# Performance work log

Hardware: AMD Instinct MI355X
Metric: run time of the kernel (lower is better)

The kernel has to match this reference:

```python
import jax, jax.numpy as jnp
import numpy as np

T, B, S = 8, 4, 2048
LAT, SYM, NC = 1024, 256, 512


def setup_inputs() -> dict:
    key = jax.random.key(0)
    ks = jax.random.split(key, 16)
    inp = {
        "token_state": jax.random.normal(ks[0], (B, S, LAT), jnp.float32),
        "bus_symbols": jax.random.normal(ks[1], (T, B, S, SYM), jnp.float32),
        "bus_indices": jax.random.randint(ks[2], (T, B, S), 0, NC),
        "bus_outputs": jax.random.normal(ks[3], (T, B, S, LAT), jnp.float32),
        "bus_mask": jnp.zeros((T,), jnp.bool_),
        # parameters (stored as (in, out) matrices)
        "Wq": jax.random.normal(ks[4], (SYM, 1), jnp.float32) / np.sqrt(SYM),
        "bq": jnp.zeros((1,), jnp.float32),
        "Wread": jax.random.normal(ks[5], (2 * LAT, LAT), jnp.float32) / np.sqrt(2 * LAT),
        "bread": jnp.zeros((LAT,), jnp.float32),
        "Wsym": jax.random.normal(ks[6], (LAT, SYM), jnp.float32) / np.sqrt(LAT),
        "bsym": jnp.zeros((SYM,), jnp.float32),
        "Wc1": jax.random.normal(ks[7], (LAT + SYM, LAT), jnp.float32) / np.sqrt(LAT + SYM),
        "bc1": jnp.zeros((LAT,), jnp.float32),
        "Wc2": jax.random.normal(ks[8], (LAT, LAT), jnp.float32) / np.sqrt(LAT),
        "bc2": jnp.zeros((LAT,), jnp.float32),
        "codebook": jax.random.normal(ks[9], (NC, SYM), jnp.float32),
    }
    return inp


def reference(token_state, bus_symbols, bus_indices, bus_outputs, bus_mask,
              Wq, bq, Wread, bread, Wsym, bsym, Wc1, bc1, Wc2, bc2, codebook):
    Tm, Bb, Ss, Dsym = bus_symbols.shape
    N = Bb * Ss
    syms = bus_symbols.reshape(Tm, N, Dsym)          # [T, N, SYM]
    outs = bus_outputs.reshape(Tm, N, -1)            # [T, N, LAT]

    # top-1 bus message routing
    relevance = (syms @ Wq + bq)[..., 0]             # [T, N]
    top_msg_idx = jnp.argmax(relevance, axis=0)      # [N]
    chosen = jnp.take_along_axis(outs, top_msg_idx[None, :, None], axis=0)[0]  # [N, LAT]
    bus_context = chosen.reshape(Bb, Ss, -1)

    z = jnp.concatenate([token_state, bus_context], axis=-1)
    z_read = z @ Wread + bread                       # [B, S, LAT]
    raw_symbol = z_read @ Wsym + bsym                # [B, S, SYM]

    # VQ: cdist argmin (squared distance has same argmin)
    flat = raw_symbol.reshape(-1, Dsym)              # [N, SYM]
    d2 = (jnp.sum(flat * flat, axis=1, keepdims=True)
          - 2.0 * flat @ codebook.T
          + jnp.sum(codebook * codebook, axis=1)[None, :])  # [N, NC]
    indices = jnp.argmin(d2, axis=-1)                # [N]
    quantized = codebook[indices].reshape(Bb, Ss, Dsym)

    h = jax.nn.relu(jnp.concatenate([z_read, quantized], axis=-1) @ Wc1 + bc1)
    node_output = h @ Wc2 + bc2 + token_state

    used_counts = jnp.zeros((Tm,), jnp.int32).at[top_msg_idx].add(1)
    keep_mask = used_counts == 0
    return node_output, quantized, indices.reshape(Bb, Ss), keep_mask
```

## Files before the change

### kernel.cpp

```cpp
#include <hip/hip_runtime.h>
#include <hip/hip_bf16.h>

#define DEVI __device__ __forceinline__

namespace {

constexpr int T_   = 8;
constexpr int NTOK = 8192;
constexpr int LAT  = 1024;
constexpr int SYM  = 256;
constexpr int NC   = 512;
constexpr float TAU = 0.6f;

typedef short short8 __attribute__((ext_vector_type(8)));
typedef float floatx4 __attribute__((ext_vector_type(4)));

DEVI unsigned short f2bf(float f){
  union { float f; unsigned u; } v; v.f = f;
  return (unsigned short)((v.u + 0x7fffu + ((v.u >> 16) & 1u)) >> 16);
}

DEVI void gload_lds16(const void* g, void* l){
  __builtin_amdgcn_global_load_lds((const __attribute__((address_space(1))) void*)g,
                                   (__attribute__((address_space(3))) void*)l, 16, 0, 0);
}

__global__ void route_k(const float* __restrict__ syms, const float* __restrict__ Wq,
                        int* __restrict__ top, int* __restrict__ counts){
  int gt = blockIdx.x * blockDim.x + threadIdx.x;
  int wid = gt >> 6, lane = gt & 63;
  if (wid >= NTOK) return;
  float4 wq = *(const float4*)(Wq + lane * 4);
  float best = -INFINITY; int bt = 0;
  for (int t = 0; t < T_; ++t){
    float4 s = *(const float4*)(syms + ((size_t)t * NTOK + wid) * SYM + lane * 4);
    float p = s.x*wq.x + s.y*wq.y + s.z*wq.z + s.w*wq.w;
    #pragma unroll
    for (int off = 32; off; off >>= 1) p += __shfl_down(p, off, 64);
    p = __shfl(p, 0, 64);
    if (p > best){ best = p; bt = t; }
  }
  if (lane == 0){ top[wid] = bt; atomicAdd(&counts[bt], 1); }
}

__global__ void cbt_k(const float* __restrict__ cb, float* __restrict__ cbT,
                      const int* __restrict__ counts, float* __restrict__ out_mask){
  int i = blockIdx.x * blockDim.x + threadIdx.x;
  if (i < NC * SYM){ int c = i / SYM, k = i % SYM; cbT[k * NC + c] = cb[i]; }
  if (blockIdx.x == 0 && threadIdx.x < T_)
    out_mask[threadIdx.x] = (counts[threadIdx.x] == 0) ? 1.0f : 0.0f;
}

__global__ void cnorm_k(const float* __restrict__ cb, const float* __restrict__ bsym,
                        float* __restrict__ cnorm, float* __restrict__ svec,
                        const float* __restrict__ bread, const float* __restrict__ Wsym,
                        float* __restrict__ rb){
  if (blockIdx.x == NC/4){
    int t = threadIdx.x;
    float a0=0.f,a1=0.f,a2=0.f,a3=0.f;
    for (int k = 0; k < LAT; k += 4){
      a0 += bread[k+0] * Wsym[(size_t)(k+0) * SYM + t];
      a1 += bread[k+1] * Wsym[(size_t)(k+1) * SYM + t];
      a2 += bread[k+2] * Wsym[(size_t)(k+2) * SYM + t];
      a3 += bread[k+3] * Wsym[(size_t)(k+3) * SYM + t];
    }
    rb[t] = bsym[t] + ((a0+a1)+(a2+a3));
    return;
  }
  int gt = blockIdx.x * blockDim.x + threadIdx.x;
  int wid = gt >> 6, lane = gt & 63;
  if (wid >= NC) return;
  float4 v = *(const float4*)(cb + (size_t)wid * SYM + lane * 4);
  float4 b = *(const float4*)(bsym + lane * 4);
  float p = v.x*v.x + v.y*v.y + v.z*v.z + v.w*v.w;
  float q = v.x*(v.x-2.f*b.x) + v.y*(v.y-2.f*b.y) + v.z*(v.z-2.f*b.z) + v.w*(v.w-2.f*b.w);
  #pragma unroll
  for (int off = 32; off; off >>= 1){ p += __shfl_down(p, off, 64); q += __shfl_down(q, off, 64); }
  if (lane == 0){ cnorm[wid] = p; svec[wid] = q; }
}

__global__ void t32multi_k(const float* __restrict__ Wread, unsigned short* __restrict__ WreadT,
                           const float* __restrict__ Wc1,   unsigned short* __restrict__ Wc1T,
                           const float* __restrict__ Wc2,   unsigned short* __restrict__ Wc2T){
  __shared__ float tile[32][33];
  int b = blockIdx.x;
  const float* in; unsigned short* out; int R, C, t;
  if (b < 2048){ in = Wread; out = WreadT; R = 2*LAT; C = LAT; t = b; }
  else if (b < 2048+1280){ in = Wc1; out = Wc1T; R = LAT+SYM; C = LAT; t = b - 2048; }
  else { in = Wc2; out = Wc2T; R = LAT; C = LAT; t = b - 3328; }
  int bx = t % 32, by = t / 32;
  int r0 = by * 32, c0 = bx * 32;
  int tid = threadIdx.x;
  int tx = tid & 31, ty = tid >> 5;
  #pragma unroll
  for (int j = 0; j < 4; ++j)
    tile[ty + j*8][tx] = in[(size_t)(r0 + ty + j*8) * C + c0 + tx];
  __syncthreads();
  #pragma unroll
  for (int j = 0; j < 4; ++j)
    out[(size_t)(c0 + ty + j*8) * R + r0 + tx] = f2bf(tile[tx][ty + j*8]);
}

__global__ void pack_az(const float* __restrict__ ts, const float* __restrict__ bus,
                        const int* __restrict__ top, unsigned short* __restrict__ Az){
  int id = blockIdx.x * blockDim.x + threadIdx.x;
  int m = id >> 9, c = (id & 511) * 4;
  const float* src = (c < LAT) ? (ts + (size_t)m * LAT + c)
                               : (bus + ((size_t)top[m] * NTOK + m) * LAT + (c - LAT));
  float4 v = *(const float4*)src;
  ushort4 o; o.x = f2bf(v.x); o.y = f2bf(v.y); o.z = f2bf(v.z); o.w = f2bf(v.w);
  *(ushort4*)(Az + (size_t)m * (2*LAT) + c) = o;
}

template<int BM, int BN, int BK, int TM, int TN, int TB>
__global__ __launch_bounds__((BM/TM)*(BN/TN))
void gemm_f32(const float* __restrict__ A, const float* __restrict__ Bm,
              float* __restrict__ Cf, unsigned short* __restrict__ Ct,
              int M, int N, int K)
{
  constexpr int NT  = (BM/TM)*(BN/TN);
  constexpr int BMp = BM + 4, BNp = BN + 4;
  constexpr int KV  = BK / 4;
  constexpr int NLA = BM * KV;
  constexpr int NLB = (BK * BN) / 4;
  __shared__ float As[BK][BMp];
  __shared__ float Bs[BK][BNp];
  const int tid = threadIdx.x;
  const int tx = tid % (BN / TN), ty = tid / (BN / TN);
  const int m0 = blockIdx.x * BM, n0 = blockIdx.y * BN;
  float acc[TM][TN] = {};
  for (int k0 = 0; k0 < K; k0 += BK){
    for (int q = tid; q < NLA; q += NT){
      int m = q / KV, kq = (q % KV) * 4;
      float4 v = *(const float4*)(A + (size_t)(m0+m) * K + k0 + kq);
      As[kq+0][m] = v.x; As[kq+1][m] = v.y; As[kq+2][m] = v.z; As[kq+3][m] = v.w;
    }
    for (int q = tid; q < NLB; q += NT){
      int k = q / (BN/4), n4 = (q % (BN/4)) * 4;
      *(float4*)&Bs[k][n4] = *(const float4*)(Bm + (size_t)(k0+k) * N + n0 + n4);
    }
    __syncthreads();
    #pragma unroll
    for (int k = 0; k < BK; ++k){
      float a[TM], b[TN];
      #pragma unroll
      for (int i = 0; i < TM; ++i) a[i] = As[k][ty*TM + i];
      #pragma unroll
      for (int j = 0; j < TN; ++j) b[j] = Bs[k][tx*TN + j];
      #pragma unroll
      for (int i = 0; i < TM; ++i)
        #pragma unroll
        for (int j = 0; j < TN; ++j) acc[i][j] += a[i] * b[j];
    }
    __syncthreads();
  }
  #pragma unroll
  for (int i = 0; i < TM; ++i)
    #pragma unroll
    for (int j = 0; j < TN; ++j){
      if constexpr (TB){
        Ct[(size_t)(n0 + tx*TN + j) * M + m0 + ty*TM + i] = f2bf(acc[i][j]);
      } else {
        Cf[(size_t)(m0 + ty*TM + i) * N + n0 + tx*TN + j] = acc[i][j];
      }
    }
}

constexpr int A_PLAIN = 0, A_CAT = 1;
constexpr int EP_ZH = 0, EP_VQ = 1, EP_RELU = 2, EP_OUT = 3;

template<int ASRC, int EPI>
__global__ __launch_bounds__(256)
void mgemm(const unsigned short* __restrict__ A, const unsigned short* __restrict__ A2,
           const unsigned short* __restrict__ BT, const float* __restrict__ bias,
           const float* __restrict__ resid,
           unsigned short* __restrict__ Cb, float* __restrict__ Cf,
           int N, int K, int asplit)
{
  __shared__ unsigned short As[128*32];
  __shared__ unsigned short Bs[128*32];
  const int tid  = threadIdx.x;
  const int wave = tid >> 6, lane = tid & 63;
  const int wy = wave >> 1, wx = wave & 1;
  const int lq = lane >> 4, lr = lane & 15;

  const int nwg  = gridDim.x * gridDim.y;
  const int orig = blockIdx.y * gridDim.x + blockIdx.x;
  const int dec  = (orig & 7) * (nwg >> 3) + (orig >> 3);
  const int bx   = dec % gridDim.x, by = dec / gridDim.x;
  const int m0 = by * 128, n0 = bx * 128;

  floatx4 acc[4][4] = {};

  for (int k0 = 0; k0 < K; k0 += 32){
    #pragma unroll
    for (int c = 0; c < 2; ++c){
      int chunk = tid + c*256;
      int mrel = chunk >> 2, kc = (chunk & 3) * 8;
      int gk = k0 + kc;
      const unsigned short* srcA;
      if constexpr (ASRC == A_CAT){
        if (gk < asplit) srcA = A  + (size_t)(m0+mrel) * asplit + gk;
        else             srcA = A2 + (size_t)(m0+mrel) * (K-asplit) + (gk-asplit);
      } else {
        srcA = A + (size_t)(m0+mrel) * K + gk;
      }
      gload_lds16(srcA, &As[(c*256 + wave*64) * 8]);
      gload_lds16(BT + (size_t)(n0+mrel) * K + gk, &Bs[(c*256 + wave*64) * 8]);
    }
    __syncthreads();
    short8 af[4], bf[4];
    #pragma unroll
    for (int i = 0; i < 4; ++i){
      af[i] = *(const short8*)&As[(wy*64 + i*16 + lr)*32 + lq*8];
      bf[i] = *(const short8*)&Bs[(wx*64 + i*16 + lr)*32 + lq*8];
    }
    #pragma unroll
    for (int i = 0; i < 4; ++i)
      #pragma unroll
      for (int j = 0; j < 4; ++j)
        acc[i][j] = __builtin_amdgcn_mfma_f32_16x16x32_bf16(af[i], bf[j], acc[i][j], 0, 0, 0);
    __syncthreads();
  }

  #pragma unroll
  for (int i = 0; i < 4; ++i){
    #pragma unroll
    for (int j = 0; j < 4; ++j){
      int gn = n0 + wx*64 + j*16 + lr;
      #pragma unroll
      for (int r = 0; r < 4; ++r){
        int gm = m0 + wy*64 + i*16 + lq*4 + r;
        float v = acc[i][j][r];
        if constexpr (EPI == EP_ZH){
          Cb[(size_t)gm * N + gn] = f2bf(v + bias[gn]);
        } else if constexpr (EPI == EP_VQ){
          Cf[(size_t)gm * N + gn] = bias[gn] - 2.f * v;
        } else if constexpr (EPI == EP_RELU){
          float u = v + bias[gn];
          Cb[(size_t)gm * N + gn] = f2bf(u > 0.f ? u : 0.f);
        } else {
          Cf[(size_t)gm * N + gn] = v + bias[gn] + resid[(size_t)gm * N + gn];
        }
      }
    }
  }
}

__global__ void vq_k(const float* __restrict__ scores, const float* __restrict__ cb,
                     float* __restrict__ out_q, float* __restrict__ out_idx,
                     unsigned short* __restrict__ q_h,
                     int* __restrict__ rcount, int* __restrict__ rlist){
  int gt = blockIdx.x * blockDim.x + threadIdx.x;
  int wid = gt >> 6, lane = gt & 63;
  if (wid >= NTOK) return;
  const float* row = scores + (size_t)wid * NC;
  float v1 = INFINITY, v2 = INFINITY; int i1 = 0x7fffffff;
  #pragma unroll
  for (int i = 0; i < NC/64; ++i){
    int c = i*64 + lane;
    float v = row[c];
    if (v < v1){ v2 = v1; v1 = v; i1 = c; } else v2 = fminf(v2, v);
  }
  #pragma unroll
  for (int off = 32; off; off >>= 1){
    float ov1 = __shfl_down(v1, off, 64);
    int   oi1 = __shfl_down(i1, off, 64);
    float ov2 = __shfl_down(v2, off, 64);
    float rest;
    if (ov1 < v1 || (ov1 == v1 && oi1 < i1)){ rest = v1; v1 = ov1; i1 = oi1; }
    else rest = ov1;
    v2 = fminf(fminf(v2, ov2), rest);
  }
  i1 = __shfl(i1, 0, 64);
  if (lane == 0){
    out_idx[wid] = (float)i1;
    if (__shfl(v2, 0, 64) - __shfl(v1, 0, 64) < TAU){
      int p = atomicAdd(rcount, 1); rlist[p] = wid;
    }
  }
  float4 cv = *(const float4*)(cb + (size_t)i1 * SYM + lane * 4);
  *(float4*)(out_q + (size_t)wid * SYM + lane * 4) = cv;
  ushort4 qh; qh.x = f2bf(cv.x); qh.y = f2bf(cv.y); qh.z = f2bf(cv.z); qh.w = f2bf(cv.w);
  *(ushort4*)(q_h + (size_t)wid * SYM + lane * 4) = qh;
}

constexpr int RT = 4;

__global__ __launch_bounds__(256)
void repair_k(const int* __restrict__ rcount, const int* __restrict__ rlist,
              const int* __restrict__ top,
              const float* __restrict__ ts, const float* __restrict__ bus,
              const float* __restrict__ Wcomb, const float* __restrict__ rb,
              const float* __restrict__ cb, const float* __restrict__ cnorm,
              float* __restrict__ out_q, float* __restrict__ out_idx,
              unsigned short* __restrict__ q_h){
  __shared__ float a[RT][2*LAT];
  __shared__ float raw[RT][SYM];
  __shared__ float pv[RT][4];
  __shared__ int   pi[RT][4];
  __shared__ int   fidx[RT];
  int tid = threadIdx.x;
  int lane = tid & 63, wave = tid >> 6;
  int cnt = *rcount;
  int nchunk = (cnt + RT - 1) / RT;
  for (int ch = blockIdx.x; ch < nchunk; ch += gridDim.x){
    int base = ch * RT;
    int nt = min(RT, cnt - base);
    for (int q = tid; q < nt * 512; q += 256){
      int t = q >> 9, c = (q & 511) * 4;
      int m = rlist[base + t];
      int tp = top[m];
      float4 v = (c < LAT) ? *(const float4*)(ts + (size_t)m * LAT + c)
                           : *(const float4*)(bus + ((size_t)tp * NTOK + m) * LAT + (c - LAT));
      *(float4*)&a[t][c] = v;
    }
    __syncthreads();
    float acc0[RT], acc1[RT], acc2[RT], acc3[RT];
    #pragma unroll
    for (int t = 0; t < RT; ++t){ acc0[t]=0.f; acc1[t]=0.f; acc2[t]=0.f; acc3[t]=0.f; }
    for (int k = 0; k < 2*LAT; k += 4){
      float w0 = Wcomb[(size_t)(k+0) * SYM + tid];
      float w1 = Wcomb[(size_t)(k+1) * SYM + tid];
      float w2 = Wcomb[(size_t)(k+2) * SYM + tid];
      float w3 = Wcomb[(size_t)(k+3) * SYM + tid];
      #pragma unroll
      for (int t = 0; t < RT; ++t){
        float4 av = *(const float4*)&a[t][k];
        acc0[t] += av.x * w0; acc1[t] += av.y * w1;
        acc2[t] += av.z * w2; acc3[t] += av.w * w3;
      }
    }
    #pragma unroll
    for (int t = 0; t < RT; ++t)
      raw[t][tid] = rb[tid] + ((acc0[t] + acc1[t]) + (acc2[t] + acc3[t]));
    __syncthreads();
    float bv[RT]; int bi[RT];
    #pragma unroll
    for (int t = 0; t < RT; ++t){ bv[t] = INFINITY; bi[t] = 0x7fffffff; }
    #pragma unroll
    for (int cc = 0; cc < 2; ++cc){
      int c = tid + cc * 256;
      const float* cr = cb + (size_t)c * SYM;
      float d[RT] = {};
      for (int j = 0; j < SYM; j += 4){
        float4 cv = *(const float4*)(cr + j);
        #pragma unroll
        for (int t = 0; t < RT; ++t){
          float4 rv4 = *(const float4*)&raw[t][j];
          d[t] += rv4.x*cv.x + rv4.y*cv.y + rv4.z*cv.z + rv4.w*cv.w;
        }
      }
      #pragma unroll
      for (int t = 0; t < RT; ++t){
        float s = cnorm[c] - 2.f * d[t];
        if (s < bv[t] || (s == bv[t] && c < bi[t])){ bv[t] = s; bi[t] = c; }
      }
    }
    #pragma unroll
    for (int t = 0; t < RT; ++t){
      float v = bv[t]; int i = bi[t];
      #pragma unroll
      for (int off = 32; off; off >>= 1){
        float ov = __shfl_down(v, off, 64);
        int   oi = __shfl_down(i, off, 64);
        if (ov < v || (ov == v && oi < i)){ v = ov; i = oi; }
      }
      if (lane == 0){ pv[t][wave] = v; pi[t][wave] = i; }
    }
    __syncthreads();
    if (tid < nt){
      float v = pv[tid][0]; int i = pi[tid][0];
      #pragma unroll
      for (int w = 1; w < 4; ++w){
        if (pv[tid][w] < v || (pv[tid][w] == v && pi[tid][w] < i)){ v = pv[tid][w]; i = pi[tid][w]; }
      }
      fidx[tid] = i;
      out_idx[rlist[base + tid]] = (float)i;
    }
    __syncthreads();
    for (int t = 0; t < nt; ++t){
      int m = rlist[base + t];
      int idx = fidx[t];
      float cvv = cb[(size_t)idx * SYM + tid];
      out_q[(size_t)m * SYM + tid] = cvv;
      q_h[(size_t)m * SYM + tid] = f2bf(cvv);
    }
    __syncthreads();
  }
}

}

extern "C" void kernel_launch(void* const* d_in, const int* in_sizes, int n_in,
                              void* d_out, int out_size, void* d_ws, size_t ws_size,
                              hipStream_t stream){
  const float* token_state = (const float*)d_in[0];
  const float* bus_symbols = (const float*)d_in[1];
  const float* bus_outputs = (const float*)d_in[3];
  const float* Wq    = (const float*)d_in[5];
  const float* Wread = (const float*)d_in[7];
  const float* bread = (const float*)d_in[8];
  const float* Wsym  = (const float*)d_in[9];
  const float* bsym  = (const float*)d_in[10];
  const float* Wc1   = (const float*)d_in[11];
  const float* bc1   = (const float*)d_in[12];
  const float* Wc2   = (const float*)d_in[13];
  const float* bc2   = (const float*)d_in[14];
  const float* codebook = (const float*)d_in[15];

  float* out_node = (float*)d_out;
  float* out_quant= out_node + (size_t)NTOK * LAT;
  float* out_idx  = out_quant + (size_t)NTOK * SYM;
  float* out_mask = out_idx + NTOK;

  char* W = (char*)d_ws; size_t off = 0;
  auto alloc = [&](size_t bytes)->char*{ char* p = W + off; off = (off + bytes + 255) & ~(size_t)255; return p; };
  int*   top     = (int*)alloc(NTOK*4);
  char*  zeroed  = alloc(256);
  int*   counts  = (int*)zeroed;
  int*   rcount  = (int*)(zeroed + 128);
  int*   rlist   = (int*)alloc(NTOK*4);
  float* cbT     = (float*)alloc((size_t)SYM*NC*4);
  float* cnorm   = (float*)alloc(NC*4);
  float* svec    = (float*)alloc(NC*4);
  float* rb      = (float*)alloc(SYM*4);
  float* Wcomb   = (float*)alloc((size_t)2*LAT*SYM*4);
  unsigned short* WreadT = (unsigned short*)alloc((size_t)LAT*2*LAT*2);
  unsigned short* Wc1T   = (unsigned short*)alloc((size_t)LAT*(LAT+SYM)*2);
  unsigned short* Wc2T   = (unsigned short*)alloc((size_t)LAT*LAT*2);
  unsigned short* WfuseT = (unsigned short*)alloc((size_t)NC*LAT*2);
  unsigned short* z_h    = (unsigned short*)alloc((size_t)NTOK*LAT*2);
  unsigned short* q_h    = (unsigned short*)alloc((size_t)NTOK*SYM*2);
  unsigned short* h_h    = (unsigned short*)alloc((size_t)NTOK*LAT*2);
  char* az_region        = alloc((size_t)NTOK*2*LAT*2);
  unsigned short* A_z    = (unsigned short*)az_region;
  float* scores          = (float*)az_region;

  hipMemsetAsync(zeroed, 0, 256, stream);

  route_k<<<NTOK/4, 256, 0, stream>>>(bus_symbols, Wq, top, counts);
  cbt_k<<<(NC*SYM)/256, 256, 0, stream>>>(codebook, cbT, counts, out_mask);
  cnorm_k<<<NC/4 + 1, 256, 0, stream>>>(codebook, bsym, cnorm, svec, bread, Wsym, rb);

  gemm_f32<64,64,8,4,4,1><<<dim3(LAT/64, NC/64), 256, 0, stream>>>(
      Wsym, cbT, nullptr, WfuseT, LAT, NC, SYM);
  gemm_f32<32,64,8,2,4,0><<<dim3(2*LAT/32, SYM/64), 256, 0, stream>>>(
      Wread, Wsym, Wcomb, nullptr, 2*LAT, SYM, LAT);
  t32multi_k<<<2048+1280+1024, 256, 0, stream>>>(Wread, WreadT, Wc1, Wc1T, Wc2, Wc2T);

  pack_az<<<(NTOK*512)/256, 256, 0, stream>>>(token_state, bus_outputs, top, A_z);

  mgemm<A_PLAIN, EP_ZH><<<dim3(LAT/128, NTOK/128), 256, 0, stream>>>(
      A_z, nullptr, WreadT, bread, nullptr, z_h, nullptr, LAT, 2*LAT, 0);
  mgemm<A_PLAIN, EP_VQ><<<dim3(NC/128, NTOK/128), 256, 0, stream>>>(
      z_h, nullptr, WfuseT, svec, nullptr, nullptr, scores, NC, LAT, 0);

  vq_k<<<NTOK/4, 256, 0, stream>>>(scores, codebook, out_quant, out_idx, q_h, rcount, rlist);
  repair_k<<<512, 256, 0, stream>>>(rcount, rlist, top, token_state, bus_outputs,
                                    Wcomb, rb, codebook, cnorm, out_quant, out_idx, q_h);

  mgemm<A_CAT, EP_RELU><<<dim3(LAT/128, NTOK/128), 256, 0, stream>>>(
      z_h, q_h, Wc1T, bc1, nullptr, h_h, nullptr, LAT, LAT+SYM, LAT);
  mgemm<A_PLAIN, EP_OUT><<<dim3(LAT/128, NTOK/128), 256, 0, stream>>>(
      h_h, nullptr, Wc2T, bc2, token_state, nullptr, out_node, LAT, LAT, 0);
}
```

Baseline: 905.9 us.

## Fuse routing with A-pack and merge weight-prep kernels into one launch

Routing now packs each token's bf16 A row (token state plus chosen bus output) in the same wave, so the separate pack kernel and its re-read of top indices go away. All weight preprocessing (Wfuse GEMM reading the codebook directly without a transposed copy, Wcomb GEMM, the three transposes, codebook norms, read bias) is merged into one block-dispatched kernel. The keep-mask write moves into the VQ kernel. This cuts launch count and lets the small prep jobs run side by side, at the cost of uneven per-block work and strided codebook loads in the Wfuse tile.

```diff
diff --git a/kernel.cpp b/kernel.cpp
--- a/kernel.cpp
+++ b/kernel.cpp
@@ -25,11 +25,12 @@
                                    (__attribute__((address_space(3))) void*)l, 16, 0, 0);
 }
 
-__global__ void route_k(const float* __restrict__ syms, const float* __restrict__ Wq,
-                        int* __restrict__ top, int* __restrict__ counts){
+__global__ void routepack_k(const float* __restrict__ syms, const float* __restrict__ Wq,
+                            const float* __restrict__ ts, const float* __restrict__ bus,
+                            int* __restrict__ top, int* __restrict__ counts,
+                            unsigned short* __restrict__ Az){
   int gt = blockIdx.x * blockDim.x + threadIdx.x;
   int wid = gt >> 6, lane = gt & 63;
-  if (wid >= NTOK) return;
   float4 wq = *(const float4*)(Wq + lane * 4);
   float best = -INFINITY; int bt = 0;
   for (int t = 0; t < T_; ++t){
@@ -41,35 +42,126 @@
     if (p > best){ best = p; bt = t; }
   }
   if (lane == 0){ top[wid] = bt; atomicAdd(&counts[bt], 1); }
-}
-
-__global__ void cbt_k(const float* __restrict__ cb, float* __restrict__ cbT,
-                      const int* __restrict__ counts, float* __restrict__ out_mask){
-  int i = blockIdx.x * blockDim.x + threadIdx.x;
-  if (i < NC * SYM){ int c = i / SYM, k = i % SYM; cbT[k * NC + c] = cb[i]; }
-  if (blockIdx.x == 0 && threadIdx.x < T_)
-    out_mask[threadIdx.x] = (counts[threadIdx.x] == 0) ? 1.0f : 0.0f;
-}
-
-__global__ void cnorm_k(const float* __restrict__ cb, const float* __restrict__ bsym,
-                        float* __restrict__ cnorm, float* __restrict__ svec,
-                        const float* __restrict__ bread, const float* __restrict__ Wsym,
-                        float* __restrict__ rb){
-  if (blockIdx.x == NC/4){
-    int t = threadIdx.x;
-    float a0=0.f,a1=0.f,a2=0.f,a3=0.f;
-    for (int k = 0; k < LAT; k += 4){
-      a0 += bread[k+0] * Wsym[(size_t)(k+0) * SYM + t];
-      a1 += bread[k+1] * Wsym[(size_t)(k+1) * SYM + t];
-      a2 += bread[k+2] * Wsym[(size_t)(k+2) * SYM + t];
-      a3 += bread[k+3] * Wsym[(size_t)(k+3) * SYM + t];
-    }
-    rb[t] = bsym[t] + ((a0+a1)+(a2+a3));
-    return;
-  }
-  int gt = blockIdx.x * blockDim.x + threadIdx.x;
-  int wid = gt >> 6, lane = gt & 63;
-  if (wid >= NC) return;
+  const float* tsrow  = ts  + (size_t)wid * LAT;
+  const float* busrow = bus + ((size_t)bt * NTOK + wid) * LAT;
+  unsigned short* az  = Az + (size_t)wid * (2*LAT);
+  #pragma unroll
+  for (int i = 0; i < 4; ++i){
+    int c = (i*64 + lane) * 4;
+    float4 v = *(const float4*)(tsrow + c);
+    ushort4 o; o.x = f2bf(v.x); o.y = f2bf(v.y); o.z = f2bf(v.z); o.w = f2bf(v.w);
+    *(ushort4*)(az + c) = o;
+    float4 w = *(const float4*)(busrow + c);
+    ushort4 p2; p2.x = f2bf(w.x); p2.y = f2bf(w.y); p2.z = f2bf(w.z); p2.w = f2bf(w.w);
+    *(ushort4*)(az + LAT + c) = p2;
+  }
+}
+
+constexpr int MP_WFUSE = 128, MP_WCOMB = 384, MP_T32 = 4736, MP_CNORM = 4864;
+
+DEVI void dev_wfuse(int tb, int tid, float* smem,
+                    const float* __restrict__ Wsym, const float* __restrict__ cb,
+                    unsigned short* __restrict__ WfuseT){
+  float (*As)[68] = (float(*)[68])smem;
+  float (*Bs)[68] = (float(*)[68])(smem + 544);
+  const int bxm = tb & 15, byn = tb >> 4;
+  const int m0 = bxm * 64, n0 = byn * 64;
+  const int tx = tid & 15, ty = tid >> 4;
+  float acc[4][4] = {};
+  for (int k0 = 0; k0 < SYM; k0 += 8){
+    if (tid < 128){
+      int m = tid >> 1, kq = (tid & 1) * 4;
+      float4 v = *(const float4*)(Wsym + (size_t)(m0+m) * SYM + k0 + kq);
+      As[kq+0][m] = v.x; As[kq+1][m] = v.y; As[kq+2][m] = v.z; As[kq+3][m] = v.w;
+    }
+    {
+      int n = tid >> 2, kk = (tid & 3) * 2;
+      float2 v = *(const float2*)(cb + (size_t)(n0+n) * SYM + k0 + kk);
+      Bs[kk+0][n] = v.x; Bs[kk+1][n] = v.y;
+    }
+    __syncthreads();
+    #pragma unroll
+    for (int k = 0; k < 8; ++k){
+      float a[4], b[4];
+      #pragma unroll
+      for (int i = 0; i < 4; ++i) a[i] = As[k][ty*4 + i];
+      #pragma unroll
+      for (int j = 0; j < 4; ++j) b[j] = Bs[k][tx*4 + j];
+      #pragma unroll
+      for (int i = 0; i < 4; ++i)
+        #pragma unroll
+        for (int j = 0; j < 4; ++j) acc[i][j] += a[i] * b[j];
+    }
+    __syncthreads();
+  }
+  #pragma unroll
+  for (int i = 0; i < 4; ++i)
+    #pragma unroll
+    for (int j = 0; j < 4; ++j)
+      WfuseT[(size_t)(n0 + tx*4 + j) * LAT + m0 + ty*4 + i] = f2bf(acc[i][j]);
+}
+
+DEVI void dev_wcomb(int tb, int tid, float* smem,
+                    const float* __restrict__ Wread, const float* __restrict__ Wsym,
+                    float* __restrict__ Wcomb){
+  float (*As)[68] = (float(*)[68])smem;
+  float (*Bs)[68] = (float(*)[68])(smem + 544);
+  const int bxm = tb & 63, byn = tb >> 6;
+  const int m0 = bxm * 32, n0 = byn * 64;
+  const int tx = tid & 15, ty = tid >> 4;
+  float acc[2][4] = {};
+  for (int k0 = 0; k0 < LAT; k0 += 8){
+    if (tid < 64){
+      int m = tid >> 1, kq = (tid & 1) * 4;
+      float4 v = *(const float4*)(Wread + (size_t)(m0+m) * LAT + k0 + kq);
+      As[kq+0][m] = v.x; As[kq+1][m] = v.y; As[kq+2][m] = v.z; As[kq+3][m] = v.w;
+    }
+    if (tid < 128){
+      int k = tid >> 4, n4 = (tid & 15) * 4;
+      *(float4*)&Bs[k][n4] = *(const float4*)(Wsym + (size_t)(k0+k) * SYM + n0 + n4);
+    }
+    __syncthreads();
+    #pragma unroll
+    for (int k = 0; k < 8; ++k){
+      float a[2], b[4];
+      #pragma unroll
+      for (int i = 0; i < 2; ++i) a[i] = As[k][ty*2 + i];
+      #pragma unroll
+      for (int j = 0; j < 4; ++j) b[j] = Bs[k][tx*4 + j];
+      #pragma unroll
+      for (int i = 0; i < 2; ++i)
+        #pragma unroll
+        for (int j = 0; j < 4; ++j) acc[i][j] += a[i] * b[j];
+    }
+    __syncthreads();
+  }
+  #pragma unroll
+  for (int i = 0; i < 2; ++i)
+    #pragma unroll
+    for (int j = 0; j < 4; ++j)
+      Wcomb[(size_t)(m0 + ty*2 + i) * SYM + n0 + tx*4 + j] = acc[i][j];
+}
+
+DEVI void dev_t32(int t, int tid, float* smem,
+                  const float* __restrict__ in, unsigned short* __restrict__ out,
+                  int R, int C){
+  float (*tile)[33] = (float(*)[33])smem;
+  int bx = t % 32, by = t / 32;
+  int r0 = by * 32, c0 = bx * 32;
+  int tx = tid & 31, ty = tid >> 5;
+  #pragma unroll
+  for (int j = 0; j < 4; ++j)
+    tile[ty + j*8][tx] = in[(size_t)(r0 + ty + j*8) * C + c0 + tx];
+  __syncthreads();
+  #pragma unroll
+  for (int j = 0; j < 4; ++j)
+    out[(size_t)(c0 + ty + j*8) * R + r0 + tx] = f2bf(tile[tx][ty + j*8]);
+}
+
+DEVI void dev_cnorm(int lb, int tid, const float* __restrict__ cb,
+                    const float* __restrict__ bsym,
+                    float* __restrict__ cnorm, float* __restrict__ svec){
+  int wid = lb * 4 + (tid >> 6), lane = tid & 63;
   float4 v = *(const float4*)(cb + (size_t)wid * SYM + lane * 4);
   float4 b = *(const float4*)(bsym + lane * 4);
   float p = v.x*v.x + v.y*v.y + v.z*v.z + v.w*v.w;
@@ -79,91 +171,45 @@
   if (lane == 0){ cnorm[wid] = p; svec[wid] = q; }
 }
 
-__global__ void t32multi_k(const float* __restrict__ Wread, unsigned short* __restrict__ WreadT,
-                           const float* __restrict__ Wc1,   unsigned short* __restrict__ Wc1T,
-                           const float* __restrict__ Wc2,   unsigned short* __restrict__ Wc2T){
-  __shared__ float tile[32][33];
-  int b = blockIdx.x;
-  const float* in; unsigned short* out; int R, C, t;
-  if (b < 2048){ in = Wread; out = WreadT; R = 2*LAT; C = LAT; t = b; }
-  else if (b < 2048+1280){ in = Wc1; out = Wc1T; R = LAT+SYM; C = LAT; t = b - 2048; }
-  else { in = Wc2; out = Wc2T; R = LAT; C = LAT; t = b - 3328; }
-  int bx = t % 32, by = t / 32;
-  int r0 = by * 32, c0 = bx * 32;
-  int tid = threadIdx.x;
-  int tx = tid & 31, ty = tid >> 5;
-  #pragma unroll
-  for (int j = 0; j < 4; ++j)
-    tile[ty + j*8][tx] = in[(size_t)(r0 + ty + j*8) * C + c0 + tx];
-  __syncthreads();
-  #pragma unroll
-  for (int j = 0; j < 4; ++j)
-    out[(size_t)(c0 + ty + j*8) * R + r0 + tx] = f2bf(tile[tx][ty + j*8]);
-}
-
-__global__ void pack_az(const float* __restrict__ ts, const float* __restrict__ bus,
-                        const int* __restrict__ top, unsigned short* __restrict__ Az){
-  int id = blockIdx.x * blockDim.x + threadIdx.x;
-  int m = id >> 9, c = (id & 511) * 4;
-  const float* src = (c < LAT) ? (ts + (size_t)m * LAT + c)
-                               : (bus + ((size_t)top[m] * NTOK + m) * LAT + (c - LAT));
-  float4 v = *(const float4*)src;
-  ushort4 o; o.x = f2bf(v.x); o.y = f2bf(v.y); o.z = f2bf(v.z); o.w = f2bf(v.w);
-  *(ushort4*)(Az + (size_t)m * (2*LAT) + c) = o;
-}
-
-template<int BM, int BN, int BK, int TM, int TN, int TB>
-__global__ __launch_bounds__((BM/TM)*(BN/TN))
-void gemm_f32(const float* __restrict__ A, const float* __restrict__ Bm,
-              float* __restrict__ Cf, unsigned short* __restrict__ Ct,
-              int M, int N, int K)
-{
-  constexpr int NT  = (BM/TM)*(BN/TN);
-  constexpr int BMp = BM + 4, BNp = BN + 4;
-  constexpr int KV  = BK / 4;
-  constexpr int NLA = BM * KV;
-  constexpr int NLB = (BK * BN) / 4;
-  __shared__ float As[BK][BMp];
-  __shared__ float Bs[BK][BNp];
-  const int tid = threadIdx.x;
-  const int tx = tid % (BN / TN), ty = tid / (BN / TN);
-  const int m0 = blockIdx.x * BM, n0 = blockIdx.y * BN;
-  float acc[TM][TN] = {};
-  for (int k0 = 0; k0 < K; k0 += BK){
-    for (int q = tid; q < NLA; q += NT){
-      int m = q / KV, kq = (q % KV) * 4;
-      float4 v = *(const float4*)(A + (size_t)(m0+m) * K + k0 + kq);
-      As[kq+0][m] = v.x; As[kq+1][m] = v.y; As[kq+2][m] = v.z; As[kq+3][m] = v.w;
-    }
-    for (int q = tid; q < NLB; q += NT){
-      int k = q / (BN/4), n4 = (q % (BN/4)) * 4;
-      *(float4*)&Bs[k][n4] = *(const float4*)(Bm + (size_t)(k0+k) * N + n0 + n4);
-    }
-    __syncthreads();
-    #pragma unroll
-    for (int k = 0; k < BK; ++k){
-      float a[TM], b[TN];
-      #pragma unroll
-      for (int i = 0; i < TM; ++i) a[i] = As[k][ty*TM + i];
-      #pragma unroll
-      for (int j = 0; j < TN; ++j) b[j] = Bs[k][tx*TN + j];
-      #pragma unroll
-      for (int i = 0; i < TM; ++i)
-        #pragma unroll
-        for (int j = 0; j < TN; ++j) acc[i][j] += a[i] * b[j];
-    }
-    __syncthreads();
-  }
-  #pragma unroll
-  for (int i = 0; i < TM; ++i)
-    #pragma unroll
-    for (int j = 0; j < TN; ++j){
-      if constexpr (TB){
-        Ct[(size_t)(n0 + tx*TN + j) * M + m0 + ty*TM + i] = f2bf(acc[i][j]);
-      } else {
-        Cf[(size_t)(m0 + ty*TM + i) * N + n0 + tx*TN + j] = acc[i][j];
-      }
-    }
+DEVI void dev_rbias(int tid, const float* __restrict__ bread,
+                    const float* __restrict__ Wsym, const float* __restrict__ bsym,
+                    float* __restrict__ rb){
+  float a0=0.f,a1=0.f,a2=0.f,a3=0.f;
+  for (int k = 0; k < LAT; k += 4){
+    a0 += bread[k+0] * Wsym[(size_t)(k+0) * SYM + tid];
+    a1 += bread[k+1] * Wsym[(size_t)(k+1) * SYM + tid];
+    a2 += bread[k+2] * Wsym[(size_t)(k+2) * SYM + tid];
+    a3 += bread[k+3] * Wsym[(size_t)(k+3) * SYM + tid];
+  }
+  rb[tid] = bsym[tid] + ((a0+a1)+(a2+a3));
+}
+
+__global__ __launch_bounds__(256)
+void megaprep_k(const float* __restrict__ Wsym, const float* __restrict__ cb,
+                unsigned short* __restrict__ WfuseT,
+                const float* __restrict__ Wread, float* __restrict__ Wcomb,
+                unsigned short* __restrict__ WreadT,
+                const float* __restrict__ Wc1, unsigned short* __restrict__ Wc1T,
+                const float* __restrict__ Wc2, unsigned short* __restrict__ Wc2T,
+                const float* __restrict__ bsym, float* __restrict__ cnorm,
+                float* __restrict__ svec,
+                const float* __restrict__ bread, float* __restrict__ rb){
+  __shared__ float smem[1088];
+  int b = blockIdx.x, tid = threadIdx.x;
+  if (b < MP_WFUSE){
+    dev_wfuse(b, tid, smem, Wsym, cb, WfuseT);
+  } else if (b < MP_WCOMB){
+    dev_wcomb(b - MP_WFUSE, tid, smem, Wread, Wsym, Wcomb);
+  } else if (b < MP_T32){
+    int t = b - MP_WCOMB;
+    if (t < 2048)      dev_t32(t,        tid, smem, Wread, WreadT, 2*LAT, LAT);
+    else if (t < 3328) dev_t32(t - 2048, tid, smem, Wc1,   Wc1T,   LAT+SYM, LAT);
+    else               dev_t32(t - 3328, tid, smem, Wc2,   Wc2T,   LAT,  LAT);
+  } else if (b < MP_CNORM){
+    dev_cnorm(b - MP_T32, tid, cb, bsym, cnorm, svec);
+  } else {
+    dev_rbias(tid, bread, Wsym, bsym, rb);
+  }
 }
 
 constexpr int A_PLAIN = 0, A_CAT = 1;
@@ -250,7 +296,10 @@
 __global__ void vq_k(const float* __restrict__ scores, const float* __restrict__ cb,
                      float* __restrict__ out_q, float* __restrict__ out_idx,
                      unsigned short* __restrict__ q_h,
-                     int* __restrict__ rcount, int* __restrict__ rlist){
+                     int* __restrict__ rcount, int* __restrict__ rlist,
+                     const int* __restrict__ counts, float* __restrict__ out_mask){
+  if (blockIdx.x == 0 && threadIdx.x < T_)
+    out_mask[threadIdx.x] = (counts[threadIdx.x] == 0) ? 1.0f : 0.0f;
   int gt = blockIdx.x * blockDim.x + threadIdx.x;
   int wid = gt >> 6, lane = gt & 63;
   if (wid >= NTOK) return;
@@ -421,7 +470,6 @@
   int*   counts  = (int*)zeroed;
   int*   rcount  = (int*)(zeroed + 128);
   int*   rlist   = (int*)alloc(NTOK*4);
-  float* cbT     = (float*)alloc((size_t)SYM*NC*4);
   float* cnorm   = (float*)alloc(NC*4);
   float* svec    = (float*)alloc(NC*4);
   float* rb      = (float*)alloc(SYM*4);
@@ -439,24 +487,19 @@
 
   hipMemsetAsync(zeroed, 0, 256, stream);
 
-  route_k<<<NTOK/4, 256, 0, stream>>>(bus_symbols, Wq, top, counts);
-  cbt_k<<<(NC*SYM)/256, 256, 0, stream>>>(codebook, cbT, counts, out_mask);
-  cnorm_k<<<NC/4 + 1, 256, 0, stream>>>(codebook, bsym, cnorm, svec, bread, Wsym, rb);
-
-  gemm_f32<64,64,8,4,4,1><<<dim3(LAT/64, NC/64), 256, 0, stream>>>(
-      Wsym, cbT, nullptr, WfuseT, LAT, NC, SYM);
-  gemm_f32<32,64,8,2,4,0><<<dim3(2*LAT/32, SYM/64), 256, 0, stream>>>(
-      Wread, Wsym, Wcomb, nullptr, 2*LAT, SYM, LAT);
-  t32multi_k<<<2048+1280+1024, 256, 0, stream>>>(Wread, WreadT, Wc1, Wc1T, Wc2, Wc2T);
-
-  pack_az<<<(NTOK*512)/256, 256, 0, stream>>>(token_state, bus_outputs, top, A_z);
+  routepack_k<<<NTOK/4, 256, 0, stream>>>(bus_symbols, Wq, token_state, bus_outputs,
+                                          top, counts, A_z);
+  megaprep_k<<<MP_CNORM + 1, 256, 0, stream>>>(
+      Wsym, codebook, WfuseT, Wread, Wcomb, WreadT, Wc1, Wc1T, Wc2, Wc2T,
+      bsym, cnorm, svec, bread, rb);
 
   mgemm<A_PLAIN, EP_ZH><<<dim3(LAT/128, NTOK/128), 256, 0, stream>>>(
       A_z, nullptr, WreadT, bread, nullptr, z_h, nullptr, LAT, 2*LAT, 0);
   mgemm<A_PLAIN, EP_VQ><<<dim3(NC/128, NTOK/128), 256, 0, stream>>>(
       z_h, nullptr, WfuseT, svec, nullptr, nullptr, scores, NC, LAT, 0);
 
-  vq_k<<<NTOK/4, 256, 0, stream>>>(scores, codebook, out_quant, out_idx, q_h, rcount, rlist);
+  vq_k<<<NTOK/4, 256, 0, stream>>>(scores, codebook, out_quant, out_idx, q_h,
+                                   rcount, rlist, counts, out_mask);
   repair_k<<<512, 256, 0, stream>>>(rcount, rlist, top, token_state, bus_outputs,
                                     Wcomb, rb, codebook, cnorm, out_quant, out_idx, q_h);
 
```

New measurement: 797.9 us. 1.14x faster.
